# Kernel optimization log

Hardware: AMD Instinct MI355X
Metric: run time of the kernel (lower is better)

The kernel has to match this reference:

```python
import jax, jax.numpy as jnp
import numpy as np

B, S, H = 8, 4096, 2048
HINT, WS, STRIDE = 4, 16, 8
MLP_H = 64


def _window_starts():
    # Mirrors the torch loop: break when the window is shorter than window_size//2.
    starts = []
    for s in range(0, S, STRIDE):
        e = min(s + WS, S)
        if e - s < WS // 2:
            break
        starts.append(s)
    return np.asarray(starts, dtype=np.int32)  # [W] = [512]


def setup_inputs() -> dict:
    key = jax.random.key(0)
    k1, k2, k3, k4, k5 = jax.random.split(key, 5)
    return {
        "hidden_states": jax.random.normal(k1, (B, S, H), jnp.float32),
        "attention_mask": jax.random.randint(k2, (B, S), 0, 2).astype(jnp.int32),
        "hint_features": jax.random.normal(k3, (B, S, HINT), jnp.float32),
        "W1": jax.random.normal(k4, (H + HINT, MLP_H), jnp.float32) * 0.02,
        "b1": jnp.zeros((MLP_H,), jnp.float32),
        "W2": jax.random.normal(k5, (MLP_H, 1), jnp.float32) * 0.02,
        "b2": jnp.zeros((1,), jnp.float32),
    }


def reference(hidden_states, attention_mask, hint_features, W1, b1, W2, b2):
    starts = jnp.asarray(_window_starts())               # [W]
    idx = starts[:, None] + jnp.arange(WS)               # [W, ws]
    pos_valid = (idx < S).astype(jnp.float32)            # [W, ws]  (pads past seq end)
    idxc = jnp.minimum(idx, S - 1)

    # [B, W, ws] combined attention + in-bounds mask
    mask = attention_mask[:, idxc].astype(jnp.float32) * pos_valid[None]
    denom = jnp.clip(jnp.sum(mask, axis=-1, keepdims=True), 1.0, None)  # [B, W, 1]

    # Gather overlapping windows once, pool with a single einsum each.
    win_h = hidden_states[:, idxc]                        # [B, W, ws, H]
    win_f = hint_features[:, idxc]                        # [B, W, ws, HINT]
    pooled_h = jnp.einsum('bwk,bwkh->bwh', mask, win_h) / denom
    pooled_f = jnp.einsum('bwk,bwkh->bwh', mask, win_f) / denom
    pooled = jnp.concatenate([pooled_h, pooled_f], axis=-1)  # [B, W, H+HINT]

    # MLP (dropout is identity at inference); torch GELU default = exact erf.
    h = jax.nn.gelu(pooled @ W1 + b1, approximate=False)
    window_logits = (h @ W2 + b2)[..., 0]                 # [B, W]
    window_mask = (jnp.sum(mask, axis=-1) > 0).astype(jnp.float32)  # [B, W]
    return window_logits, window_mask
```

## Files before the change

kernel.cpp:

```cpp
#include <hip/hip_runtime.h>
#include <math.h>

#define B_      8
#define S_      4096
#define H_      2048
#define HINT_   4
#define WS_     16
#define STRIDE_ 8
#define MLPH_   64
#define NW_     512
#define WPB_    8
#define ROWS_   72
#define KT_     68
#define KPAD_   2176
#define LDK_    2184
#define NT_     4

typedef float  floatx4 __attribute__((ext_vector_type(4)));
typedef short  shortx8 __attribute__((ext_vector_type(8)));

__device__ __forceinline__ unsigned short f2b(float x) {
    unsigned u = __float_as_uint(x);
    u += 0x7FFFu + ((u >> 16) & 1u);
    return (unsigned short)(u >> 16);
}

__global__ void prep_w1(const float* __restrict__ W1, unsigned short* __restrict__ W1B) {
    const int blk  = blockIdx.x;
    const int nt   = blk / KT_;
    const int kt   = blk % KT_;
    const int lane = threadIdx.x;
    const int n     = nt * 16 + (lane & 15);
    const int kbase = kt * 32 + (lane >> 4) * 8;
    unsigned short tmp[8];
#pragma unroll
    for (int j = 0; j < 8; ++j) {
        const int k = kbase + j;
        const float v = (k < (H_ + HINT_)) ? W1[(size_t)k * MLPH_ + n] : 0.0f;
        tmp[j] = f2b(v);
    }
    *(uint4*)(W1B + (((size_t)nt * KT_ + kt) * 64 + lane) * 8) = *(const uint4*)tmp;
}

__global__ __launch_bounds__(512) void wbh_kernel(
    const float* __restrict__ hidden,
    const int*   __restrict__ amask,
    const float* __restrict__ hintf,
    const float* __restrict__ b1,
    const float* __restrict__ W2,
    const float* __restrict__ b2,
    const unsigned short* __restrict__ W1B,
    float* __restrict__ out)
{
    __shared__ unsigned short pooledLds[16 * LDK_];
    __shared__ float amLds[ROWS_];
    __shared__ float hintLds[ROWS_ * HINT_];
    __shared__ float rinvLds[WPB_];
    __shared__ float partLds[WPB_ * 68];

    const int tid   = threadIdx.x;
    const int bid   = blockIdx.x;
    const int b     = bid >> 6;
    const int chunk = bid & 63;
    const int w0    = chunk * WPB_;
    const int s0    = chunk * (WPB_ * STRIDE_);

    {
        unsigned int* p = (unsigned int*)pooledLds;
        const int n4 = 16 * LDK_ / 2;
        for (int i = tid; i < n4; i += 512) p[i] = 0u;
    }
    if (tid < ROWS_) {
        const int p = s0 + tid;
        amLds[tid] = (p < S_) ? (float)amask[b * S_ + p] : 0.0f;
    }
    if (tid < ROWS_ * HINT_) {
        const int rr = tid >> 2;
        const int p  = s0 + rr;
        hintLds[tid] = (p < S_) ? hintf[((size_t)b * S_ + p) * HINT_ + (tid & 3)] : 0.0f;
    }
    __syncthreads();

    if (tid < WPB_) {
        float s = 0.f;
#pragma unroll
        for (int k = 0; k < WS_; ++k) s += amLds[tid * STRIDE_ + k];
        rinvLds[tid] = 1.0f / fmaxf(s, 1.0f);
        out[(size_t)(B_ * NW_) + (size_t)b * NW_ + w0 + tid] = (s > 0.f) ? 1.0f : 0.0f;
    }
    __syncthreads();

    const int c0 = tid * 4;
    const float* rowBase = hidden + ((size_t)b * S_ + s0) * H_ + c0;

    floatx4 prev = (floatx4){0.f, 0.f, 0.f, 0.f};
#pragma unroll
    for (int g = 0; g <= WPB_; ++g) {
        floatx4 cur = (floatx4){0.f, 0.f, 0.f, 0.f};
#pragma unroll
        for (int k = 0; k < STRIDE_; ++k) {
            const int rr = g * STRIDE_ + k;
            const float amv = amLds[rr];
            if (amv != 0.0f) {
                cur += *(const floatx4*)(rowBase + (size_t)rr * H_);
            }
        }
        if (g >= 1) {
            const int w = g - 1;
            const floatx4 s = prev + cur;
            const float r = rinvLds[w];
            unsigned short q[4];
            q[0] = f2b(s.x * r); q[1] = f2b(s.y * r);
            q[2] = f2b(s.z * r); q[3] = f2b(s.w * r);
            *(uint2*)(&pooledLds[w * LDK_ + c0]) = *(const uint2*)q;
        }
        prev = cur;
    }

    if (tid < WPB_ * HINT_) {
        const int w = tid >> 2, hc = tid & 3;
        float s = 0.f;
#pragma unroll
        for (int k = 0; k < WS_; ++k) {
            const int rr = w * STRIDE_ + k;
            s += amLds[rr] * hintLds[rr * HINT_ + hc];
        }
        pooledLds[w * LDK_ + H_ + hc] = f2b(s * rinvLds[w]);
    }
    __syncthreads();

    const int wid  = tid >> 6;
    const int lane = tid & 63;
    if (wid < NT_) {
        floatx4 dacc = (floatx4){0.f, 0.f, 0.f, 0.f};
        const unsigned short* aBase = pooledLds + (lane & 15) * LDK_ + (lane >> 4) * 8;
        const unsigned short* bBase = W1B + (((size_t)wid * KT_) * 64 + lane) * 8;
#pragma unroll 4
        for (int kt = 0; kt < KT_; ++kt) {
            const shortx8 af = *(const shortx8*)(aBase + kt * 32);
            const shortx8 bf = *(const shortx8*)(bBase + (size_t)kt * 64 * 8);
            dacc = __builtin_amdgcn_mfma_f32_16x16x32_bf16(af, bf, dacc, 0, 0, 0);
        }
        const int j   = wid * 16 + (lane & 15);
        const float b1v = b1[j];
        const float w2v = W2[j];
        const int m0  = (lane >> 4) * 4;
        if (m0 < WPB_) {
#pragma unroll
            for (int r = 0; r < 4; ++r) {
                const float a  = dacc[r] + b1v;
                const float gv = 0.5f * a * (1.0f + erff(a * 0.70710678118654752f));
                partLds[(m0 + r) * 68 + j] = gv * w2v;
            }
        }
    }
    __syncthreads();

    if (tid < WPB_) {
        float s = b2[0];
#pragma unroll
        for (int j = 0; j < MLPH_; ++j) s += partLds[tid * 68 + j];
        out[(size_t)b * NW_ + w0 + tid] = s;
    }
}

extern "C" void kernel_launch(void* const* d_in, const int* in_sizes, int n_in,
                              void* d_out, int out_size, void* d_ws, size_t ws_size,
                              hipStream_t stream) {
    const float* hidden = (const float*)d_in[0];
    const int*   amask  = (const int*)d_in[1];
    const float* hintf  = (const float*)d_in[2];
    const float* W1     = (const float*)d_in[3];
    const float* b1     = (const float*)d_in[4];
    const float* W2     = (const float*)d_in[5];
    const float* b2     = (const float*)d_in[6];
    float* out          = (float*)d_out;

    unsigned short* W1B = (unsigned short*)d_ws;

    prep_w1<<<NT_ * KT_, 64, 0, stream>>>(W1, W1B);
    wbh_kernel<<<B_ * (NW_ / WPB_), 512, 0, stream>>>(
        hidden, amask, hintf, b1, W2, b2, W1B, out);
}
```

Baseline: 349.2 us.

## Split MFMA K-loop across all waves, shrink LDS, and use mask bitsets

The kernel now splits the K dimension of the W1 matmul across all eight waves instead of using four. Partial sums are combined in LDS, and GELU plus the W2 dot product run as a wave-wide shuffle reduction. The pooled LDS buffer is halved to the 8 real rows, only its padding tail is zeroed, and launch bounds ask for higher occupancy. The per-row mask test becomes a scalar bitmask read through readfirstlane, and block IDs are remapped across batches. The aim is less serial MFMA latency, less LDS zeroing and better occupancy, but the MFMA A operand now reads duplicated rows for lanes 8-15, which looks odd.

```diff
diff --git a/kernel.cpp b/kernel.cpp
--- a/kernel.cpp
+++ b/kernel.cpp
@@ -15,6 +15,7 @@
 #define KPAD_   2176
 #define LDK_    2184
 #define NT_     4
+#define PLD_    66
 
 typedef float  floatx4 __attribute__((ext_vector_type(4)));
 typedef short  shortx8 __attribute__((ext_vector_type(8)));
@@ -42,7 +43,7 @@
     *(uint4*)(W1B + (((size_t)nt * KT_ + kt) * 64 + lane) * 8) = *(const uint4*)tmp;
 }
 
-__global__ __launch_bounds__(512) void wbh_kernel(
+__global__ __launch_bounds__(512, 8) void wbh_kernel(
     const float* __restrict__ hidden,
     const int*   __restrict__ amask,
     const float* __restrict__ hintf,
@@ -52,23 +53,24 @@
     const unsigned short* __restrict__ W1B,
     float* __restrict__ out)
 {
-    __shared__ unsigned short pooledLds[16 * LDK_];
+    __shared__ unsigned short pooledLds[WPB_ * LDK_];
     __shared__ float amLds[ROWS_];
     __shared__ float hintLds[ROWS_ * HINT_];
     __shared__ float rinvLds[WPB_];
-    __shared__ float partLds[WPB_ * 68];
+    __shared__ unsigned amBitsLds[WPB_ + 1];
+    __shared__ float partLds[WPB_ * 2 * PLD_];
 
-    const int tid   = threadIdx.x;
-    const int bid   = blockIdx.x;
-    const int b     = bid >> 6;
-    const int chunk = bid & 63;
+    const int tid = threadIdx.x;
+    const int bid = blockIdx.x;
+    const int gid   = (bid & 7) * 64 + (bid >> 3);
+    const int b     = gid >> 6;
+    const int chunk = gid & 63;
     const int w0    = chunk * WPB_;
     const int s0    = chunk * (WPB_ * STRIDE_);
 
-    {
-        unsigned int* p = (unsigned int*)pooledLds;
-        const int n4 = 16 * LDK_ / 2;
-        for (int i = tid; i < n4; i += 512) p[i] = 0u;
+    if (tid < 8 * 62) {
+        const int row = tid / 62, cc = tid % 62;
+        *(unsigned*)&pooledLds[row * LDK_ + 2052 + cc * 2] = 0u;
     }
     if (tid < ROWS_) {
         const int p = s0 + tid;
@@ -88,6 +90,13 @@
         rinvLds[tid] = 1.0f / fmaxf(s, 1.0f);
         out[(size_t)(B_ * NW_) + (size_t)b * NW_ + w0 + tid] = (s > 0.f) ? 1.0f : 0.0f;
     }
+    if (tid < WPB_ + 1) {
+        unsigned bits = 0;
+#pragma unroll
+        for (int k = 0; k < STRIDE_; ++k)
+            bits |= (amLds[tid * STRIDE_ + k] != 0.0f ? 1u : 0u) << k;
+        amBitsLds[tid] = bits;
+    }
     __syncthreads();
 
     const int c0 = tid * 4;
@@ -96,13 +105,13 @@
     floatx4 prev = (floatx4){0.f, 0.f, 0.f, 0.f};
 #pragma unroll
     for (int g = 0; g <= WPB_; ++g) {
+        const unsigned bits =
+            (unsigned)__builtin_amdgcn_readfirstlane((int)amBitsLds[g]);
         floatx4 cur = (floatx4){0.f, 0.f, 0.f, 0.f};
 #pragma unroll
         for (int k = 0; k < STRIDE_; ++k) {
-            const int rr = g * STRIDE_ + k;
-            const float amv = amLds[rr];
-            if (amv != 0.0f) {
-                cur += *(const floatx4*)(rowBase + (size_t)rr * H_);
+            if (bits & (1u << k)) {
+                cur += *(const floatx4*)(rowBase + (size_t)(g * STRIDE_ + k) * H_);
             }
         }
         if (g >= 1) {
@@ -131,36 +140,39 @@
 
     const int wid  = tid >> 6;
     const int lane = tid & 63;
-    if (wid < NT_) {
+    const int nt   = wid & 3;
+    const int kh   = wid >> 2;
+    {
         floatx4 dacc = (floatx4){0.f, 0.f, 0.f, 0.f};
-        const unsigned short* aBase = pooledLds + (lane & 15) * LDK_ + (lane >> 4) * 8;
-        const unsigned short* bBase = W1B + (((size_t)wid * KT_) * 64 + lane) * 8;
+        const unsigned short* aBase =
+            pooledLds + (lane & 7) * LDK_ + (lane >> 4) * 8 + kh * 34 * 32;
+        const unsigned short* bBase =
+            W1B + (((size_t)nt * KT_ + kh * 34) * 64 + lane) * 8;
 #pragma unroll 4
-        for (int kt = 0; kt < KT_; ++kt) {
+        for (int kt = 0; kt < 34; ++kt) {
             const shortx8 af = *(const shortx8*)(aBase + kt * 32);
             const shortx8 bf = *(const shortx8*)(bBase + (size_t)kt * 64 * 8);
             dacc = __builtin_amdgcn_mfma_f32_16x16x32_bf16(af, bf, dacc, 0, 0, 0);
         }
-        const int j   = wid * 16 + (lane & 15);
-        const float b1v = b1[j];
-        const float w2v = W2[j];
-        const int m0  = (lane >> 4) * 4;
-        if (m0 < WPB_) {
+        if (lane < 32) {
+            const int m0 = (lane >> 4) * 4;
+            const int j  = nt * 16 + (lane & 15);
 #pragma unroll
-            for (int r = 0; r < 4; ++r) {
-                const float a  = dacc[r] + b1v;
-                const float gv = 0.5f * a * (1.0f + erff(a * 0.70710678118654752f));
-                partLds[(m0 + r) * 68 + j] = gv * w2v;
-            }
+            for (int r = 0; r < 4; ++r)
+                partLds[((m0 + r) * 2 + kh) * PLD_ + j] = dacc[r];
         }
     }
     __syncthreads();
 
-    if (tid < WPB_) {
-        float s = b2[0];
+    {
+        const int m = tid >> 6;
+        const int j = tid & 63;
+        const float a = partLds[(m * 2) * PLD_ + j] + partLds[(m * 2 + 1) * PLD_ + j]
+                      + b1[j];
+        float g = 0.5f * a * (1.0f + erff(a * 0.70710678118654752f)) * W2[j];
 #pragma unroll
-        for (int j = 0; j < MLPH_; ++j) s += partLds[tid * 68 + j];
-        out[(size_t)b * NW_ + w0 + tid] = s;
+        for (int off = 32; off > 0; off >>= 1) g += __shfl_down(g, off, 64);
+        if (j == 0) out[(size_t)b * NW_ + w0 + m] = g + b2[0];
     }
 }
 
```

Measured after the change: 349.2 us. No clear change (-0.0%).
